# Performance work log

Hardware: AMD Instinct MI355X
Metric: run time of the kernel (lower is better)

The kernel has to match this reference:

```python
import jax, jax.numpy as jnp
import numpy as np

B, T, C = 16, 2048, 384
E = 8          # num_experts
TOP_K = 2
CAP_F = 1.0
D_FF = 4 * C   # 1536


def setup_inputs() -> dict:
    key = jax.random.key(0)
    ks = jax.random.split(key, 10)
    s = 0.02
    return {
        "x": jax.random.normal(ks[0], (B, T, C), dtype=jnp.float32),
        "noise": jax.random.normal(ks[1], (B, T, E), dtype=jnp.float32),
        "w_route": jax.random.normal(ks[2], (C, E), dtype=jnp.float32) * s,
        "b_route": jnp.zeros((E,), dtype=jnp.float32),
        "w_noise": jax.random.normal(ks[3], (C, E), dtype=jnp.float32) * s,
        "b_noise": jnp.zeros((E,), dtype=jnp.float32),
        "w1": jax.random.normal(ks[4], (E, C, D_FF), dtype=jnp.float32) * s,
        "b1": jnp.zeros((E, D_FF), dtype=jnp.float32),
        "w2": jax.random.normal(ks[5], (E, D_FF, C), dtype=jnp.float32) * s,
        "b2": jnp.zeros((E, C), dtype=jnp.float32),
    }


def _moe_forward(x, noise, w_route, b_route, w_noise, b_noise, w1, b1, w2, b2):
    Bx, Tx, Cx = x.shape
    N = Bx * Tx
    cap = int(N * TOP_K / E * CAP_F)  # static expert capacity

    # --- NoisyTopkRouter ---
    logits = jnp.einsum('btc,ce->bte', x, w_route) + b_route
    noise_logits = jnp.einsum('btc,ce->bte', x, w_noise) + b_noise
    noisy = logits + noise * jax.nn.softplus(noise_logits)
    topv, topi = jax.lax.top_k(noisy, TOP_K)                    # [B,T,K]
    keep_mask = jnp.any(jax.nn.one_hot(topi, E, dtype=jnp.bool_), axis=-2)  # [B,T,E]
    sparse_logits = jnp.where(keep_mask, noisy, -jnp.inf)
    gating = jax.nn.softmax(sparse_logits, axis=-1)             # [B,T,E]

    # --- dispatch by top-1 expert with capacity drop (eval: dropout off) ---
    flat_x = x.reshape(N, Cx)
    flat_g = gating.reshape(N, E)
    top1 = jnp.argmax(flat_g, axis=-1)                          # [N]
    token_ids = jnp.arange(N, dtype=jnp.int32)
    out = jnp.zeros_like(flat_x)

    for i in range(E):
        mask = top1 == i                                        # [N]
        pos = jnp.cumsum(mask) - 1                              # rank within expert
        keep = mask & (pos < cap)
        slot = jnp.where(keep, pos, cap)                        # overflow -> dummy slot
        buf = jnp.zeros((cap + 1,), dtype=jnp.int32).at[slot].set(token_ids)
        idx = buf[:cap]                                         # token id per capacity slot
        valid = (jnp.arange(cap) < jnp.sum(keep))[:, None]      # [cap,1]
        xi = flat_x[idx]                                        # [cap,C] gather
        h = jnp.square(jax.nn.relu(xi @ w1[i] + b1[i]))         # ReLU^2
        yi = h @ w2[i] + b2[i]                                  # [cap,C]
        weighted = yi * flat_g[idx, i][:, None] * valid
        out = out.at[idx].add(weighted)                         # scatter-add

    return out.reshape(Bx, Tx, Cx)


def reference(x, noise, w_route, b_route, w_noise, b_noise, w1, b1, w2, b2):
    return _moe_forward(x, noise, w_route, b_route, w_noise, b_noise, w1, b1, w2, b2)
```

## Files before the change

kernel.cpp:

```cpp
#include <hip/hip_runtime.h>
#include <stdint.h>

#define E_NUM 8
#define CAP 8192
#define NTOK 32768
#define CDIM 384
#define DFF 1536
#define CNT_PAD 64

typedef unsigned short u16;
typedef __attribute__((ext_vector_type(8))) short short8;
typedef __attribute__((ext_vector_type(4))) float f32x4;

__device__ inline u16 f2bf(float f) {
    uint32_t u = __builtin_bit_cast(uint32_t, f);
    u += 0x7fffu + ((u >> 16) & 1u);
    return (u16)(u >> 16);
}

__device__ inline void gload_lds16(const void* g, void* l) {
    __builtin_amdgcn_global_load_lds(
        (const __attribute__((address_space(1))) void*)(uintptr_t)g,
        (__attribute__((address_space(3))) void*)(uint32_t)(uintptr_t)l,
        16, 0, 0);
}

__device__ inline void expert_span(const int* __restrict__ cnt, int e,
                                   int& base, int& n_e) {
    base = 0; n_e = 0;
#pragma unroll
    for (int i = 0; i < E_NUM; ++i) {
        int n = min(cnt[i * CNT_PAD], CAP);
        if (i < e) base += (n + 127) & ~127;
        else if (i == e) n_e = n;
    }
}

#define RT_TOK 64
#define RT_KC 64
#define RT_XS 68
#define RT_BLOCKS (NTOK / RT_TOK)
#define TR_BLOCKS (48 * 12 * 16)

__global__ __launch_bounds__(256, 3) void route_prep_kernel(
    const float* __restrict__ x, const float* __restrict__ noise,
    const float* __restrict__ w_route, const float* __restrict__ b_route,
    const float* __restrict__ w_noise, const float* __restrict__ b_noise,
    int* __restrict__ cnt, int* __restrict__ list, float* __restrict__ gate,
    u16* __restrict__ xbf,
    const float* __restrict__ w1, u16* __restrict__ W1t,
    const float* __restrict__ w2, u16* __restrict__ W2t)
{
    __shared__ float xs[RT_TOK * RT_XS];
    __shared__ float ws_r[CDIM * E_NUM];
    __shared__ float ws_n[CDIM * E_NUM];
    __shared__ float tile[32][33];
    int tid = threadIdx.x;
    int bid = blockIdx.x;

    if (bid >= RT_BLOCKS) {
        int b = bid - RT_BLOCKS;
        int z = b / 576;
        int rem = b % 576;
        int by = rem / 48, bx = rem % 48;
        const float* in; u16* out; int S, r0, c0;
        if (z < E_NUM) {
            in = w1 + (size_t)z * CDIM * DFF;  out = W1t + (size_t)z * CDIM * DFF;
            S = DFF;
            c0 = bx * 32; r0 = by * 32;
        } else {
            in = w2 + (size_t)(z - E_NUM) * DFF * CDIM;
            out = W2t + (size_t)(z - E_NUM) * DFF * CDIM;
            S = CDIM;
            r0 = bx * 32; c0 = by * 32;
        }
        int R = (z < E_NUM) ? CDIM : DFF;
        int tx = tid & 31, ty = tid >> 5;
#pragma unroll
        for (int i = ty; i < 32; i += 8)
            tile[i][tx] = in[(size_t)(r0 + i) * S + (c0 + tx)];
        __syncthreads();
#pragma unroll
        for (int i = ty; i < 32; i += 8)
            out[(size_t)(c0 + i) * R + (r0 + tx)] = f2bf(tile[tx][i]);
        return;
    }

    int lane = tid & 63;
    int seg = __builtin_amdgcn_readfirstlane(tid >> 6);
    int tok = tid & 63;
    int t0 = bid * RT_TOK;

#pragma unroll
    for (int i = 0; i < 3; ++i) {
        int idx = tid + i * 256;
        *(float4*)&ws_r[idx * 4] = ((const float4*)w_route)[idx];
        *(float4*)&ws_n[idx * 4] = ((const float4*)w_noise)[idx];
    }

    int srow = tid >> 4;
    int scol = (tid & 15) * 4;

    float ar[E_NUM], an[E_NUM];
#pragma unroll
    for (int e = 0; e < E_NUM; ++e) { ar[e] = 0.f; an[e] = 0.f; }

    for (int c = 0; c < CDIM / RT_KC; ++c) {
        __syncthreads();
#pragma unroll
        for (int p = 0; p < 4; ++p) {
            int row = p * 16 + srow;
            float4 v = *(const float4*)(x + (size_t)(t0 + row) * CDIM + c * RT_KC + scol);
            *(float4*)&xs[row * RT_XS + scol] = v;
            uint2 b;
            b.x = (uint32_t)f2bf(v.x) | ((uint32_t)f2bf(v.y) << 16);
            b.y = (uint32_t)f2bf(v.z) | ((uint32_t)f2bf(v.w) << 16);
            *(uint2*)(xbf + (size_t)(t0 + row) * CDIM + c * RT_KC + scol) = b;
        }
        __syncthreads();
#pragma unroll
        for (int q = 0; q < 4; ++q) {
            float4 xq = *(const float4*)&xs[tok * RT_XS + seg * 16 + q * 4];
            int kb = c * RT_KC + seg * 16 + q * 4;
#pragma unroll
            for (int jj = 0; jj < 4; ++jj) {
                const float* wrk = &ws_r[(kb + jj) * E_NUM];
                const float* wnk = &ws_n[(kb + jj) * E_NUM];
                float4 wa = *(const float4*)wrk, wb = *(const float4*)(wrk + 4);
                float4 na = *(const float4*)wnk, nb = *(const float4*)(wnk + 4);
                float xk = (jj == 0) ? xq.x : (jj == 1) ? xq.y : (jj == 2) ? xq.z : xq.w;
                ar[0] += xk * wa.x; ar[1] += xk * wa.y; ar[2] += xk * wa.z; ar[3] += xk * wa.w;
                ar[4] += xk * wb.x; ar[5] += xk * wb.y; ar[6] += xk * wb.z; ar[7] += xk * wb.w;
                an[0] += xk * na.x; an[1] += xk * na.y; an[2] += xk * na.z; an[3] += xk * na.w;
                an[4] += xk * nb.x; an[5] += xk * nb.y; an[6] += xk * nb.z; an[7] += xk * nb.w;
            }
        }
    }
    __syncthreads();
    float* part = xs;
    float* pp = part + (size_t)(seg * 64 + tok) * 16;
    *(f32x4*)&pp[0]  = (f32x4){ar[0], ar[1], ar[2], ar[3]};
    *(f32x4*)&pp[4]  = (f32x4){ar[4], ar[5], ar[6], ar[7]};
    *(f32x4*)&pp[8]  = (f32x4){an[0], an[1], an[2], an[3]};
    *(f32x4*)&pp[12] = (f32x4){an[4], an[5], an[6], an[7]};
    __syncthreads();
    if (seg == 0) {
        int t = t0 + lane;
        float sr[E_NUM], sn[E_NUM];
#pragma unroll
        for (int e = 0; e < E_NUM; ++e) { sr[e] = b_route[e]; sn[e] = b_noise[e]; }
#pragma unroll
        for (int s = 0; s < 4; ++s) {
            const float* q = part + (size_t)(s * 64 + lane) * 16;
#pragma unroll
            for (int e = 0; e < E_NUM; ++e) { sr[e] += q[e]; sn[e] += q[8 + e]; }
        }
        float nz[E_NUM];
        const float* np = noise + (size_t)t * E_NUM;
#pragma unroll
        for (int e = 0; e < E_NUM; ++e) {
            float s = sn[e];
            float sp = fmaxf(s, 0.f) + __logf(1.f + __expf(-fabsf(s)));
            nz[e] = sr[e] + np[e] * sp;
        }
        float v1 = -1e30f; int i1 = 0;
#pragma unroll
        for (int e = 0; e < E_NUM; ++e) if (nz[e] > v1) { v1 = nz[e]; i1 = e; }
        float v2 = -1e30f;
#pragma unroll
        for (int e = 0; e < E_NUM; ++e) if (e != i1 && nz[e] > v2) v2 = nz[e];
        gate[t] = 1.f / (1.f + __expf(v2 - v1));
#pragma unroll
        for (int e = 0; e < E_NUM; ++e) {
            unsigned long long m = __ballot(i1 == e);
            if (m == 0) continue;
            int cnum = __popcll(m);
            int leader = __ffsll((long long)m) - 1;
            int basec = 0;
            if (lane == leader) basec = atomicAdd(&cnt[e * CNT_PAD], cnum);
            basec = __shfl(basec, leader);
            if (i1 == e) {
                int pos = basec + __popcll(m & ((1ull << lane) - 1ull));
                if (pos < CAP) list[e * CAP + pos] = t;
            }
        }
    }
}

template <int KD, int ND, bool FFN1>
__global__ __launch_bounds__(512, 4) void gemm_kernel(
    const u16* __restrict__ A, const u16* __restrict__ Bt,
    const float* __restrict__ bias, u16* __restrict__ H, float* __restrict__ Out,
    const int* __restrict__ cnt, const int* __restrict__ list,
    const float* __restrict__ gate, const u16* __restrict__ dummy)
{
    constexpr int NT = ND / 128;
    int bid = blockIdx.x;
    int xcd = bid & 7, slot = bid >> 3;
    int n_idx = slot % NT;
    int mglob = xcd + 8 * (slot / NT);
    int e = mglob >> 6;
    int m0 = (mglob & 63) * 128;
    int base, n_e;
    expert_span(cnt, e, base, n_e);
    int pad_e = (n_e + 127) & ~127;
    if (m0 >= pad_e) return;
    const u16* Be = Bt + ((size_t)e * ND + (size_t)n_idx * 128) * KD;

    __shared__ __align__(16) u16 As[2][128 * 64];
    __shared__ __align__(16) u16 Bs[2][128 * 64];
    __shared__ int s_tok[128];

    int tid = threadIdx.x;
    int w = tid >> 6, lane = tid & 63;
    int quad = lane >> 4, l15 = lane & 15;
    int wr = w & 1;
    int wc = w >> 1;

    int srow = tid >> 3;
    int gcol = ((tid & 7) ^ (srow & 7)) * 8;

    if (FFN1) {
        if (tid < 128) {
            int rr = m0 + tid;
            s_tok[tid] = (rr < n_e) ? list[(size_t)e * CAP + rr] : -1;
        }
        __syncthreads();
    }
    const u16* Arow[2];
#pragma unroll
    for (int i = 0; i < 2; ++i) {
        int row = i * 64 + srow;
        if (FFN1) {
            int s = s_tok[row];
            Arow[i] = (s >= 0) ? A + (size_t)s * KD : dummy;
        } else {
            Arow[i] = A + (size_t)(base + m0 + row) * KD;
        }
    }

    auto stage = [&](int buf, int kb) {
#pragma unroll
        for (int i = 0; i < 2; ++i) {
            gload_lds16(Arow[i] + kb * 64 + gcol, &As[buf][i * 4096 + tid * 8]);
            gload_lds16(Be + (size_t)(i * 64 + srow) * KD + kb * 64 + gcol,
                        &Bs[buf][i * 4096 + tid * 8]);
        }
    };

    f32x4 acc[4][2];
    f32x4 zero = {0.f, 0.f, 0.f, 0.f};
#pragma unroll
    for (int a = 0; a < 4; ++a)
#pragma unroll
        for (int b = 0; b < 2; ++b) acc[a][b] = zero;

    constexpr int NK = KD / 64;
    stage(0, 0);
#pragma unroll 2
    for (int kb = 0; kb < NK; ++kb) {
        const int cur = kb & 1;
        if (kb + 1 < NK) {
            stage(cur ^ 1, kb + 1);
            asm volatile("s_waitcnt vmcnt(4)" ::: "memory");
        } else {
            asm volatile("s_waitcnt vmcnt(0)" ::: "memory");
        }
        __builtin_amdgcn_s_barrier();
        __builtin_amdgcn_sched_barrier(0);
#pragma unroll
        for (int h = 0; h < 2; ++h) {
            int pga = ((h * 4 + quad) ^ (l15 & 7)) * 8;
            short8 af[4], bf[2];
#pragma unroll
            for (int t = 0; t < 4; ++t)
                af[t] = *(const short8*)&As[cur][(wr * 64 + t * 16 + l15) * 64 + pga];
#pragma unroll
            for (int t = 0; t < 2; ++t)
                bf[t] = *(const short8*)&Bs[cur][(wc * 32 + t * 16 + l15) * 64 + pga];
#pragma unroll
            for (int mt = 0; mt < 4; ++mt)
#pragma unroll
                for (int nt = 0; nt < 2; ++nt)
                    acc[mt][nt] = __builtin_amdgcn_mfma_f32_16x16x32_bf16(
                        af[mt], bf[nt], acc[mt][nt], 0, 0, 0);
        }
        __builtin_amdgcn_sched_barrier(0);
        __builtin_amdgcn_s_barrier();
        __builtin_amdgcn_sched_barrier(0);
    }

    int n0 = n_idx * 128;
    if (FFN1) {
        u16* Hs = (u16*)&As[0][0];
#pragma unroll
        for (int mt = 0; mt < 4; ++mt) {
            int rowL = wr * 64 + mt * 16 + quad * 4;
#pragma unroll
            for (int nt = 0; nt < 2; ++nt) {
                int colL = wc * 32 + nt * 16 + l15;
                float b = bias[(size_t)e * ND + n0 + colL];
#pragma unroll
                for (int r = 0; r < 4; ++r) {
                    float v = acc[mt][nt][r] + b;
                    v = fmaxf(v, 0.f);
                    int row = rowL + r;
                    Hs[row * 128 + (colL ^ ((row & 7) << 3))] = f2bf(v * v);
                }
            }
        }
        __syncthreads();
        u16* He = H + (size_t)(base + m0) * ND + n0;
#pragma unroll
        for (int j = 0; j < 4; ++j) {
            int idx = tid + j * 512;
            int row = idx >> 4;
            int c8 = (idx & 15) * 8;
            *(f32x4*)(He + (size_t)row * ND + c8) =
                *(const f32x4*)(Hs + row * 128 + (c8 ^ ((row & 7) << 3)));
        }
    } else {
#pragma unroll
        for (int mt = 0; mt < 4; ++mt) {
            int rowL = wr * 64 + mt * 16 + quad * 4;
#pragma unroll
            for (int r = 0; r < 4; ++r) {
                int rr = m0 + rowL + r;
                if (rr < n_e) {
                    int tok = list[(size_t)e * CAP + rr];
                    float g = gate[tok];
#pragma unroll
                    for (int nt = 0; nt < 2; ++nt) {
                        int col = n0 + wc * 32 + nt * 16 + l15;
                        float v = acc[mt][nt][r] + bias[(size_t)e * ND + col];
                        Out[(size_t)tok * CDIM + col] = v * g;
                    }
                }
            }
        }
    }
}

extern "C" void kernel_launch(void* const* d_in, const int* in_sizes, int n_in,
                              void* d_out, int out_size, void* d_ws, size_t ws_size,
                              hipStream_t stream)
{
    const float* x       = (const float*)d_in[0];
    const float* noise   = (const float*)d_in[1];
    const float* w_route = (const float*)d_in[2];
    const float* b_route = (const float*)d_in[3];
    const float* w_noise = (const float*)d_in[4];
    const float* b_noise = (const float*)d_in[5];
    const float* w1      = (const float*)d_in[6];
    const float* b1      = (const float*)d_in[7];
    const float* w2      = (const float*)d_in[8];
    const float* b2      = (const float*)d_in[9];
    float* out = (float*)d_out;

    char* ws = (char*)d_ws;
    size_t off = 0;
    auto alloc = [&](size_t bytes) {
        char* p = ws + off;
        off += (bytes + 255) & ~(size_t)255;
        return p;
    };
    int*   cnt   = (int*)alloc((size_t)E_NUM * CNT_PAD * sizeof(int));
    u16*   dummy = (u16*)alloc((size_t)CDIM * 2);
    int*   list  = (int*)alloc((size_t)E_NUM * CAP * sizeof(int));
    float* gate  = (float*)alloc((size_t)NTOK * sizeof(float));
    u16*   W1t   = (u16*)alloc((size_t)E_NUM * DFF * CDIM * 2);
    u16*   W2t   = (u16*)alloc((size_t)E_NUM * CDIM * DFF * 2);
    u16*   Xbf   = (u16*)alloc((size_t)NTOK * CDIM * 2);
    size_t rows = NTOK + E_NUM * 128;
    u16*   Hb    = (u16*)alloc(rows * DFF * 2);

    hipMemsetAsync(ws, 0, (size_t)E_NUM * CNT_PAD * sizeof(int) + CDIM * 2, stream);

    route_prep_kernel<<<RT_BLOCKS + TR_BLOCKS, 256, 0, stream>>>(
        x, noise, w_route, b_route, w_noise, b_noise, cnt, list, gate, Xbf,
        w1, W1t, w2, W2t);

    gemm_kernel<CDIM, DFF, true><<<dim3((DFF / 128) * 512), 512, 0, stream>>>(
        Xbf, W1t, b1, Hb, nullptr, cnt, list, nullptr, dummy);
    gemm_kernel<DFF, CDIM, false><<<dim3((CDIM / 128) * 512), 512, 0, stream>>>(
        Hb, W2t, b2, nullptr, out, cnt, list, gate, nullptr);
}
```

Measured before the change: 301.5 us.

## Fuse routing, weight transpose and both expert GEMMs into one cooperative kernel

```diff
diff --git a/kernel.cpp b/kernel.cpp
--- a/kernel.cpp
+++ b/kernel.cpp
@@ -1,5 +1,8 @@
 #include <hip/hip_runtime.h>
+#include <hip/hip_cooperative_groups.h>
 #include <stdint.h>
+
+namespace cg = cooperative_groups;
 
 #define E_NUM 8
 #define CAP 8192
@@ -8,6 +11,10 @@
 #define DFF 1536
 #define CNT_PAD 64
 
+#define NBLK 256
+#define FFN1_TILES 6144
+#define FFN2_TILES 1536
+
 typedef unsigned short u16;
 typedef __attribute__((ext_vector_type(8))) short short8;
 typedef __attribute__((ext_vector_type(4))) float f32x4;
@@ -16,6 +23,10 @@
     uint32_t u = __builtin_bit_cast(uint32_t, f);
     u += 0x7fffu + ((u >> 16) & 1u);
     return (u16)(u >> 16);
+}
+
+__device__ inline uint32_t pk2(float a, float b) {
+    return (uint32_t)f2bf(a) | ((uint32_t)f2bf(b) << 16);
 }
 
 __device__ inline void gload_lds16(const void* g, void* l) {
@@ -36,96 +47,49 @@
     }
 }
 
-#define RT_TOK 64
-#define RT_KC 64
-#define RT_XS 68
-#define RT_BLOCKS (NTOK / RT_TOK)
-#define TR_BLOCKS (48 * 12 * 16)
-
-__global__ __launch_bounds__(256, 3) void route_prep_kernel(
+__device__ __forceinline__ void routing_slice(
+    int sl, char* smem,
     const float* __restrict__ x, const float* __restrict__ noise,
     const float* __restrict__ w_route, const float* __restrict__ b_route,
     const float* __restrict__ w_noise, const float* __restrict__ b_noise,
     int* __restrict__ cnt, int* __restrict__ list, float* __restrict__ gate,
-    u16* __restrict__ xbf,
-    const float* __restrict__ w1, u16* __restrict__ W1t,
-    const float* __restrict__ w2, u16* __restrict__ W2t)
+    u16* __restrict__ xbf)
 {
-    __shared__ float xs[RT_TOK * RT_XS];
-    __shared__ float ws_r[CDIM * E_NUM];
-    __shared__ float ws_n[CDIM * E_NUM];
-    __shared__ float tile[32][33];
+    float* xs   = (float*)smem;
+    float* part = (float*)(smem + 32768);
     int tid = threadIdx.x;
-    int bid = blockIdx.x;
-
-    if (bid >= RT_BLOCKS) {
-        int b = bid - RT_BLOCKS;
-        int z = b / 576;
-        int rem = b % 576;
-        int by = rem / 48, bx = rem % 48;
-        const float* in; u16* out; int S, r0, c0;
-        if (z < E_NUM) {
-            in = w1 + (size_t)z * CDIM * DFF;  out = W1t + (size_t)z * CDIM * DFF;
-            S = DFF;
-            c0 = bx * 32; r0 = by * 32;
-        } else {
-            in = w2 + (size_t)(z - E_NUM) * DFF * CDIM;
-            out = W2t + (size_t)(z - E_NUM) * DFF * CDIM;
-            S = CDIM;
-            r0 = bx * 32; c0 = by * 32;
-        }
-        int R = (z < E_NUM) ? CDIM : DFF;
-        int tx = tid & 31, ty = tid >> 5;
-#pragma unroll
-        for (int i = ty; i < 32; i += 8)
-            tile[i][tx] = in[(size_t)(r0 + i) * S + (c0 + tx)];
-        __syncthreads();
-#pragma unroll
-        for (int i = ty; i < 32; i += 8)
-            out[(size_t)(c0 + i) * R + (r0 + tx)] = f2bf(tile[tx][i]);
-        return;
-    }
-
     int lane = tid & 63;
     int seg = __builtin_amdgcn_readfirstlane(tid >> 6);
     int tok = tid & 63;
-    int t0 = bid * RT_TOK;
-
-#pragma unroll
-    for (int i = 0; i < 3; ++i) {
-        int idx = tid + i * 256;
-        *(float4*)&ws_r[idx * 4] = ((const float4*)w_route)[idx];
-        *(float4*)&ws_n[idx * 4] = ((const float4*)w_noise)[idx];
-    }
-
-    int srow = tid >> 4;
-    int scol = (tid & 15) * 4;
+    int t0 = sl * 64;
+    int srow = tid >> 3;
+    int scol = (tid & 7) * 8;
 
     float ar[E_NUM], an[E_NUM];
 #pragma unroll
     for (int e = 0; e < E_NUM; ++e) { ar[e] = 0.f; an[e] = 0.f; }
 
-    for (int c = 0; c < CDIM / RT_KC; ++c) {
-        __syncthreads();
-#pragma unroll
-        for (int p = 0; p < 4; ++p) {
-            int row = p * 16 + srow;
-            float4 v = *(const float4*)(x + (size_t)(t0 + row) * CDIM + c * RT_KC + scol);
-            *(float4*)&xs[row * RT_XS + scol] = v;
-            uint2 b;
-            b.x = (uint32_t)f2bf(v.x) | ((uint32_t)f2bf(v.y) << 16);
-            b.y = (uint32_t)f2bf(v.z) | ((uint32_t)f2bf(v.w) << 16);
-            *(uint2*)(xbf + (size_t)(t0 + row) * CDIM + c * RT_KC + scol) = b;
-        }
-        __syncthreads();
-#pragma unroll
-        for (int q = 0; q < 4; ++q) {
-            float4 xq = *(const float4*)&xs[tok * RT_XS + seg * 16 + q * 4];
-            int kb = c * RT_KC + seg * 16 + q * 4;
+    for (int c = 0; c < CDIM / 64; ++c) {
+        __syncthreads();
+        const float* xr = x + (size_t)(t0 + srow) * CDIM + c * 64 + scol;
+        float4 v0 = *(const float4*)xr;
+        float4 v1 = *(const float4*)(xr + 4);
+        *(float4*)&xs[srow * 68 + scol]     = v0;
+        *(float4*)&xs[srow * 68 + scol + 4] = v1;
+        uint2* xo = (uint2*)(xbf + (size_t)(t0 + srow) * CDIM + c * 64 + scol);
+        uint2 b0, b1;
+        b0.x = pk2(v0.x, v0.y); b0.y = pk2(v0.z, v0.w);
+        b1.x = pk2(v1.x, v1.y); b1.y = pk2(v1.z, v1.w);
+        xo[0] = b0; xo[1] = b1;
+        __syncthreads();
+#pragma unroll
+        for (int q = 0; q < 2; ++q) {
+            float4 xq = *(const float4*)&xs[tok * 68 + seg * 8 + q * 4];
+            int kb = c * 64 + seg * 8 + q * 4;
 #pragma unroll
             for (int jj = 0; jj < 4; ++jj) {
-                const float* wrk = &ws_r[(kb + jj) * E_NUM];
-                const float* wnk = &ws_n[(kb + jj) * E_NUM];
+                const float* wrk = w_route + (size_t)(kb + jj) * E_NUM;
+                const float* wnk = w_noise + (size_t)(kb + jj) * E_NUM;
                 float4 wa = *(const float4*)wrk, wb = *(const float4*)(wrk + 4);
                 float4 na = *(const float4*)wnk, nb = *(const float4*)(wnk + 4);
                 float xk = (jj == 0) ? xq.x : (jj == 1) ? xq.y : (jj == 2) ? xq.z : xq.w;
@@ -136,8 +100,6 @@
             }
         }
     }
-    __syncthreads();
-    float* part = xs;
     float* pp = part + (size_t)(seg * 64 + tok) * 16;
     *(f32x4*)&pp[0]  = (f32x4){ar[0], ar[1], ar[2], ar[3]};
     *(f32x4*)&pp[4]  = (f32x4){ar[4], ar[5], ar[6], ar[7]};
@@ -150,7 +112,7 @@
 #pragma unroll
         for (int e = 0; e < E_NUM; ++e) { sr[e] = b_route[e]; sn[e] = b_noise[e]; }
 #pragma unroll
-        for (int s = 0; s < 4; ++s) {
+        for (int s = 0; s < 8; ++s) {
             const float* q = part + (size_t)(s * 64 + lane) * 16;
 #pragma unroll
             for (int e = 0; e < E_NUM; ++e) { sr[e] += q[e]; sn[e] += q[8 + e]; }
@@ -187,18 +149,49 @@
     }
 }
 
+__device__ __forceinline__ void transpose_batch(
+    int tb, char* smem,
+    const float* __restrict__ w1, u16* __restrict__ W1t,
+    const float* __restrict__ w2, u16* __restrict__ W2t)
+{
+    float (*tile)[33] = (float(*)[33])smem;
+    int tid = threadIdx.x;
+    int tx = tid & 31, ty = tid >> 5;
+    for (int it = 0; it < 18; ++it) {
+        int b = tb * 18 + it;
+        int z = b / 576, rem = b % 576;
+        int by = rem / 48, bx = rem % 48;
+        const float* in; u16* out; int S, R, r0, c0;
+        if (z < E_NUM) {
+            in = w1 + (size_t)z * CDIM * DFF;  out = W1t + (size_t)z * CDIM * DFF;
+            S = DFF; R = CDIM; c0 = bx * 32; r0 = by * 32;
+        } else {
+            in = w2 + (size_t)(z - E_NUM) * DFF * CDIM;
+            out = W2t + (size_t)(z - E_NUM) * DFF * CDIM;
+            S = CDIM; R = DFF; r0 = bx * 32; c0 = by * 32;
+        }
+#pragma unroll
+        for (int i = ty; i < 32; i += 16)
+            tile[i][tx] = in[(size_t)(r0 + i) * S + (c0 + tx)];
+        __syncthreads();
+#pragma unroll
+        for (int i = ty; i < 32; i += 16)
+            out[(size_t)(c0 + i) * R + (r0 + tx)] = f2bf(tile[tx][i]);
+        __syncthreads();
+    }
+}
+
 template <int KD, int ND, bool FFN1>
-__global__ __launch_bounds__(512, 4) void gemm_kernel(
+__device__ __forceinline__ void ffn_tile(
+    int tk, char* smem, int* s_tok,
     const u16* __restrict__ A, const u16* __restrict__ Bt,
     const float* __restrict__ bias, u16* __restrict__ H, float* __restrict__ Out,
     const int* __restrict__ cnt, const int* __restrict__ list,
     const float* __restrict__ gate, const u16* __restrict__ dummy)
 {
     constexpr int NT = ND / 128;
-    int bid = blockIdx.x;
-    int xcd = bid & 7, slot = bid >> 3;
-    int n_idx = slot % NT;
-    int mglob = xcd + 8 * (slot / NT);
+    int n_idx = tk % NT;
+    int mglob = tk / NT;
     int e = mglob >> 6;
     int m0 = (mglob & 63) * 128;
     int base, n_e;
@@ -207,16 +200,14 @@
     if (m0 >= pad_e) return;
     const u16* Be = Bt + ((size_t)e * ND + (size_t)n_idx * 128) * KD;
 
-    __shared__ __align__(16) u16 As[2][128 * 64];
-    __shared__ __align__(16) u16 Bs[2][128 * 64];
-    __shared__ int s_tok[128];
+    u16* As0 = (u16*)smem;
+    u16* Bs0 = (u16*)(smem + 32768);
 
     int tid = threadIdx.x;
     int w = tid >> 6, lane = tid & 63;
     int quad = lane >> 4, l15 = lane & 15;
     int wr = w & 1;
     int wc = w >> 1;
-
     int srow = tid >> 3;
     int gcol = ((tid & 7) ^ (srow & 7)) * 8;
 
@@ -242,9 +233,9 @@
     auto stage = [&](int buf, int kb) {
 #pragma unroll
         for (int i = 0; i < 2; ++i) {
-            gload_lds16(Arow[i] + kb * 64 + gcol, &As[buf][i * 4096 + tid * 8]);
+            gload_lds16(Arow[i] + kb * 64 + gcol, &As0[buf * 8192 + i * 4096 + tid * 8]);
             gload_lds16(Be + (size_t)(i * 64 + srow) * KD + kb * 64 + gcol,
-                        &Bs[buf][i * 4096 + tid * 8]);
+                        &Bs0[buf * 8192 + i * 4096 + tid * 8]);
         }
     };
 
@@ -274,10 +265,10 @@
             short8 af[4], bf[2];
 #pragma unroll
             for (int t = 0; t < 4; ++t)
-                af[t] = *(const short8*)&As[cur][(wr * 64 + t * 16 + l15) * 64 + pga];
+                af[t] = *(const short8*)&As0[cur * 8192 + (wr * 64 + t * 16 + l15) * 64 + pga];
 #pragma unroll
             for (int t = 0; t < 2; ++t)
-                bf[t] = *(const short8*)&Bs[cur][(wc * 32 + t * 16 + l15) * 64 + pga];
+                bf[t] = *(const short8*)&Bs0[cur * 8192 + (wc * 32 + t * 16 + l15) * 64 + pga];
 #pragma unroll
             for (int mt = 0; mt < 4; ++mt)
 #pragma unroll
@@ -292,7 +283,7 @@
 
     int n0 = n_idx * 128;
     if (FFN1) {
-        u16* Hs = (u16*)&As[0][0];
+        u16* Hs = As0;
 #pragma unroll
         for (int mt = 0; mt < 4; ++mt) {
             int rowL = wr * 64 + mt * 16 + quad * 4;
@@ -339,6 +330,46 @@
             }
         }
     }
+    __syncthreads();
+}
+
+struct MegaArgs {
+    const float* x; const float* noise;
+    const float* w_route; const float* b_route;
+    const float* w_noise; const float* b_noise;
+    const float* w1; const float* b1;
+    const float* w2; const float* b2;
+    int* cnt; int* list; float* gate; u16* xbf;
+    u16* W1t; u16* W2t; u16* Hb; const u16* dummy; float* out;
+};
+
+__global__ __launch_bounds__(512, 2) void moe_coop(MegaArgs a)
+{
+    __shared__ __align__(16) char smem[65536];
+    __shared__ int s_tok[128];
+    int b = blockIdx.x;
+    cg::grid_group grid = cg::this_grid();
+
+    routing_slice(b, smem, a.x, a.noise, a.w_route, a.b_route,
+                  a.w_noise, a.b_noise, a.cnt, a.list, a.gate, a.xbf);
+    __syncthreads();
+    routing_slice(b + NBLK, smem, a.x, a.noise, a.w_route, a.b_route,
+                  a.w_noise, a.b_noise, a.cnt, a.list, a.gate, a.xbf);
+    __syncthreads();
+    transpose_batch(b, smem, a.w1, a.W1t, a.w2, a.W2t);
+    transpose_batch(b + NBLK, smem, a.w1, a.W1t, a.w2, a.W2t);
+
+    grid.sync();
+
+    for (int t = b; t < FFN1_TILES; t += NBLK)
+        ffn_tile<CDIM, DFF, true>(t, smem, s_tok, a.xbf, a.W1t, a.b1, a.Hb,
+                                  nullptr, a.cnt, a.list, nullptr, a.dummy);
+
+    grid.sync();
+
+    for (int t = b; t < FFN2_TILES; t += NBLK)
+        ffn_tile<DFF, CDIM, false>(t, smem, s_tok, a.Hb, a.W2t, a.b2, nullptr,
+                                   a.out, a.cnt, a.list, a.gate, nullptr);
 }
 
 extern "C" void kernel_launch(void* const* d_in, const int* in_sizes, int n_in,
@@ -366,6 +397,7 @@
     };
     int*   cnt   = (int*)alloc((size_t)E_NUM * CNT_PAD * sizeof(int));
     u16*   dummy = (u16*)alloc((size_t)CDIM * 2);
+    size_t zspan = off;
     int*   list  = (int*)alloc((size_t)E_NUM * CAP * sizeof(int));
     float* gate  = (float*)alloc((size_t)NTOK * sizeof(float));
     u16*   W1t   = (u16*)alloc((size_t)E_NUM * DFF * CDIM * 2);
@@ -374,14 +406,12 @@
     size_t rows = NTOK + E_NUM * 128;
     u16*   Hb    = (u16*)alloc(rows * DFF * 2);
 
-    hipMemsetAsync(ws, 0, (size_t)E_NUM * CNT_PAD * sizeof(int) + CDIM * 2, stream);
-
-    route_prep_kernel<<<RT_BLOCKS + TR_BLOCKS, 256, 0, stream>>>(
-        x, noise, w_route, b_route, w_noise, b_noise, cnt, list, gate, Xbf,
-        w1, W1t, w2, W2t);
-
-    gemm_kernel<CDIM, DFF, true><<<dim3((DFF / 128) * 512), 512, 0, stream>>>(
-        Xbf, W1t, b1, Hb, nullptr, cnt, list, nullptr, dummy);
-    gemm_kernel<DFF, CDIM, false><<<dim3((CDIM / 128) * 512), 512, 0, stream>>>(
-        Hb, W2t, b2, nullptr, out, cnt, list, gate, nullptr);
-}
+    hipMemsetAsync(ws, 0, zspan, stream);
+
+    MegaArgs args = { x, noise, w_route, b_route, w_noise, b_noise,
+                      w1, b1, w2, b2, cnt, list, gate, Xbf,
+                      W1t, W2t, Hb, dummy, out };
+    void* kparams[] = { &args };
+    hipLaunchCooperativeKernel((const void*)moe_coop, dim3(NBLK), dim3(512),
+                               kparams, 0, stream);
+}
```

Result: slower. 509.8 us (+69.1%).
